# Kernel optimization log

Measured on AMD Instinct MI355X. Metric: run time of the kernel, lower is better.

The kernel has to match this reference:

```python
import jax, jax.numpy as jnp
import numpy as np

P = 16          # patch size
IMG = 224       # image size
EPS_COMBINE = 2.220446049250313e-16  # np.finfo(float).eps
NOISE_EPS = 0.01
LOSS_COEF = 1e-2
K = 1


def _patchify(x):
    # x: [B, C, H, W] -> [B, n_patches, C*P*P] (channel-major flatten, matching conv weight layout)
    B, C, H, W = x.shape
    gh, gw = H // P, W // P
    x = x.reshape(B, C, gh, P, gw, P)
    x = x.transpose(0, 2, 4, 1, 3, 5).reshape(B, gh * gw, C * P * P)
    return x


def _cv_squared(v):
    # squared coefficient of variation; torch .var() is unbiased (ddof=1)
    return jnp.var(v, ddof=1) / (jnp.mean(v) ** 2 + 1e-10)


def _norm_cdf(v):
    return jax.scipy.stats.norm.cdf(v)


def setup_inputs() -> dict:
    key = jax.random.key(0)
    ks = jax.random.split(key, 7)
    B, E, D_IN = 64, 8, 320
    x = jax.random.normal(ks[0], (B, 3, IMG, IMG), dtype=jnp.float32)
    g = jax.random.normal(ks[1], (B, D_IN), dtype=jnp.float32)
    noise = jax.random.normal(ks[2], (B, E), dtype=jnp.float32)
    w_gate = jax.random.normal(ks[3], (D_IN, E), dtype=jnp.float32) * 0.02
    w_noise = jax.random.normal(ks[4], (D_IN, E), dtype=jnp.float32) * 0.02
    w_exp = jax.random.normal(ks[5], (E, 768, 3, P, P), dtype=jnp.float32) * 0.02
    b_exp = jnp.zeros((E, 768), dtype=jnp.float32)
    return {"x": x, "g": g, "noise": noise, "w_gate": w_gate,
            "w_noise": w_noise, "w_exp": w_exp, "b_exp": b_exp}


def reference(x, g, noise, w_gate, w_noise, w_exp, b_exp):
    B = x.shape[0]
    E = w_gate.shape[1]

    # ---- noisy top-k gating (train mode) ----
    clean_logits = g @ w_gate                                   # [B, E]
    noise_stddev = jax.nn.softplus(g @ w_noise) + NOISE_EPS     # [B, E]
    noisy_logits = clean_logits + noise * noise_stddev          # [B, E]

    top_logits, top_idx = jax.lax.top_k(noisy_logits, K + 1)    # [B, K+1]
    top_k_gates = jax.nn.softmax(top_logits[:, :K], axis=1)     # [B, K]
    gates = jnp.zeros_like(noisy_logits).at[
        jnp.arange(B)[:, None], top_idx[:, :K]].set(top_k_gates)  # [B, E]

    # load: prob each expert's noisy logit lands in top-k (differentiable balance term)
    thr_in = top_logits[:, K][:, None]       # (k+1)-th value per row
    thr_out = top_logits[:, K - 1][:, None]  # k-th value per row
    is_in = noisy_logits > thr_in
    prob = jnp.where(is_in,
                     _norm_cdf((clean_logits - thr_in) / noise_stddev),
                     _norm_cdf((clean_logits - thr_out) / noise_stddev))
    load = prob.sum(0)                                           # [E]
    importance = gates.sum(0)                                    # [E]
    loss = (_cv_squared(importance) + _cv_squared(load)) * LOSS_COEF

    # ---- experts: per-expert patch-embed conv == patchify + GEMM ----
    patches = _patchify(x)                                       # [B, 196, 768]
    wf = w_exp.reshape(E, w_exp.shape[1], -1)                    # [E, out=768, in=768]
    y_exp = jnp.einsum('bpi,eoi->ebpo', patches, wf) + b_exp[:, None, None, :]  # [E,B,196,768]

    # ---- gate-weighted combine (dense equivalent of dispatch/combine) ----
    y = jnp.einsum('be,ebpo->bpo', gates, y_exp)                 # [B, 196, 768]
    y = jnp.where(y == 0, jnp.asarray(EPS_COMBINE, y.dtype), y)  # combined[combined==0] = eps
    return y, loss
```

## Files before the change

kernel.cpp:

```cpp
#include <hip/hip_runtime.h>
#include <math.h>

typedef unsigned short u16;
typedef unsigned int   u32;

using bf16x8 = __attribute__((ext_vector_type(8))) short;
using f32x4  = __attribute__((ext_vector_type(4))) float;

#define NB   64
#define NE   8
#define DIN  320
#define NP   196
#define CK   768
#define CN   768

#define BM 128
#define BN 128
#define BK 32
#define NKT (CK / BK)

#define WCONV_BLOCKS 2304

__device__ __forceinline__ u16 f2bf(float f) {
    u32 u = __builtin_bit_cast(u32, f);
    u += 0x7fffu + ((u >> 16) & 1u);
    return (u16)(u >> 16);
}

__device__ __forceinline__ u32 pkbf(float a, float b) {
    u32 ua = (__builtin_bit_cast(u32, a) + 0x8000u) >> 16;
    u32 ub = (__builtin_bit_cast(u32, b) + 0x8000u) & 0xffff0000u;
    return ua | ub;
}

__device__ __forceinline__ void gload16(const void* g, void* l) {
    __builtin_amdgcn_global_load_lds(
        (const __attribute__((address_space(1))) void*)g,
        (__attribute__((address_space(3))) void*)l, 16, 0, 0);
}

__global__ __launch_bounds__(256) void prep1_kernel(
    const float* __restrict__ g,
    const float* __restrict__ noise,
    const float* __restrict__ w_gate,
    const float* __restrict__ w_noise,
    const float* __restrict__ w_exp,
    float* __restrict__ gCl, float* __restrict__ gSd, float* __restrict__ gNy,
    u16* __restrict__ wb)
{
    __shared__ float sW[DIN][NE + 1];
    __shared__ float sWn[DIN][NE + 1];
    const int t = threadIdx.x;
    int bid = blockIdx.x;

    if (bid < 8) {
        for (int i = t; i < DIN * NE; i += 256) {
            sW[i >> 3][i & 7]  = w_gate[i];
            sWn[i >> 3][i & 7] = w_noise[i];
        }
        __syncthreads();
        const int pair = t >> 2, q = t & 3;
        const int bl = pair >> 3, e = pair & 7;
        const int b = bid * 8 + bl;
        float cl = 0.f, nz = 0.f;
        const float* gr = g + b * DIN + q * 80;
        #pragma unroll 4
        for (int j = 0; j < 80; ++j) {
            float gv = gr[j];
            cl = fmaf(gv, sW[q * 80 + j][e], cl);
            nz = fmaf(gv, sWn[q * 80 + j][e], nz);
        }
        cl += __shfl_xor(cl, 1); cl += __shfl_xor(cl, 2);
        nz += __shfl_xor(nz, 1); nz += __shfl_xor(nz, 2);
        if (q == 0) {
            int p = b * NE + e;
            float sd = fmaxf(nz, 0.f) + log1pf(expf(-fabsf(nz))) + 0.01f;
            gCl[p] = cl; gSd[p] = sd;
            gNy[p] = fmaf(noise[p], sd, cl);
        }
        return;
    }
    bid -= 8;
    int idx = bid * 256 + t;
    const float* src = w_exp + (size_t)idx * 8;
    float4 f0 = *reinterpret_cast<const float4*>(src);
    float4 f1 = *reinterpret_cast<const float4*>(src + 4);
    uint4 o;
    o.x = (u32)f2bf(f0.x) | ((u32)f2bf(f0.y) << 16);
    o.y = (u32)f2bf(f0.z) | ((u32)f2bf(f0.w) << 16);
    o.z = (u32)f2bf(f1.x) | ((u32)f2bf(f1.y) << 16);
    o.w = (u32)f2bf(f1.z) | ((u32)f2bf(f1.w) << 16);
    *reinterpret_cast<uint4*>(wb + (size_t)idx * 8) = o;
}

__global__ __launch_bounds__(512) void gate2_kernel(
    const float* __restrict__ gCl,
    const float* __restrict__ gSd,
    const float* __restrict__ gNy,
    int* __restrict__ eid,
    float* __restrict__ loss_out)
{
    __shared__ float sNy[NB][NE];
    __shared__ float sProb[NB][NE];
    __shared__ int   sTop[NB];
    __shared__ float sImp[NE], sLoad[NE];
    const int t = threadIdx.x;
    const int b = t >> 3, e = t & 7;
    float cl = gCl[t], sd = gSd[t], ny = gNy[t];
    sNy[b][e] = ny;
    __syncthreads();
    float v1 = -1e30f, v2 = -1e30f; int i1 = 0;
    #pragma unroll
    for (int k2 = 0; k2 < NE; ++k2) {
        float v = sNy[b][k2];
        if (v > v1) { v2 = v1; v1 = v; i1 = k2; }
        else if (v > v2) { v2 = v; }
    }
    if (e == 0) { sTop[b] = i1; eid[b] = i1; }
    float thr = (ny > v2) ? v2 : v1;
    float z = (cl - thr) / sd;
    sProb[b][e] = 0.5f * (1.0f + erff(z * 0.7071067811865476f));
    __syncthreads();
    if (t < NE) {
        float imp = 0.f, ld = 0.f;
        for (int i = 0; i < NB; ++i) {
            imp += (sTop[i] == t) ? 1.0f : 0.0f;
            ld  += sProb[i][t];
        }
        sImp[t] = imp; sLoad[t] = ld;
    }
    __syncthreads();
    if (t == 0) {
        float mi = 0.f, ml = 0.f;
        for (int k2 = 0; k2 < NE; ++k2) { mi += sImp[k2]; ml += sLoad[k2]; }
        mi *= (1.0f / NE); ml *= (1.0f / NE);
        float vi = 0.f, vl = 0.f;
        for (int k2 = 0; k2 < NE; ++k2) {
            float d1 = sImp[k2] - mi;  vi += d1 * d1;
            float d2 = sLoad[k2] - ml; vl += d2 * d2;
        }
        vi *= (1.0f / (NE - 1)); vl *= (1.0f / (NE - 1));
        loss_out[0] = (vi / (mi * mi + 1e-10f) + vl / (ml * ml + 1e-10f)) * 0.01f;
    }
}

__global__ __launch_bounds__(512) void gemm_kernel(
    const float* __restrict__ x,
    const u16* __restrict__ wb,
    const float* __restrict__ b_exp,
    const int* __restrict__ eid,
    float* __restrict__ out)
{
    __shared__ char smem[2][16384];

    const int id = blockIdx.x;
    const int v  = (id & 7) * 96 + (id >> 3);
    const int b  = v / 12;
    const int rr = v % 12;
    const int m0 = (rr / 6) * BM;
    const int n0 = (rr % 6) * BN;
    const int e  = eid[b];

    const int t  = threadIdx.x;
    const int l  = t & 63;
    const int w  = t >> 6;
    const int wm = w >> 1;
    const int wn = w & 1;

    const u32 cg = (u32)((l & 3) ^ (l >> 4));
    const u16* bS = wb + (size_t)e * (CK * CN)
                  + (size_t)(n0 + (w << 4) + (l >> 2)) * CK + cg * 8;
    const u32 bLds = 8192u + ((u32)w << 10) + ((u32)l << 4);

    const int arow = t >> 2;
    int p = m0 + arow; if (p > NP - 1) p = NP - 1;
    const int gh = p / 14, gw = p % 14;
    const int seg = (t & 3) >> 1, pw0 = (t & 1) * 8;
    const float* xb = x + (size_t)b * 150528 + (gh * 16 + seg) * 224 + gw * 16 + pw0;
    const u32 wA = (u32)(arow * 64 + (((t & 3) ^ ((arow >> 2) & 3)) << 4));

    u32 aOff[2], bOff[4];
    #pragma unroll
    for (int fm = 0; fm < 2; ++fm) {
        int row = wm * 32 + fm * 16 + (l & 15);
        aOff[fm] = (u32)(row * 64) + (((u32)(l >> 4) ^ (u32)((row >> 2) & 3)) << 4);
    }
    #pragma unroll
    for (int fn = 0; fn < 4; ++fn) {
        int row = wn * 64 + fn * 16 + (l & 15);
        bOff[fn] = 8192u + (u32)(row * 64) + (((u32)(l >> 4) ^ (u32)((row >> 2) & 3)) << 4);
    }

    f32x4 acc[2][4];
    #pragma unroll
    for (int fm = 0; fm < 2; ++fm)
        #pragma unroll
        for (int fn = 0; fn < 4; ++fn)
            acc[fm][fn] = (f32x4){0.f, 0.f, 0.f, 0.f};

    char* smem0 = &smem[0][0];

    {
        float4 ra0 = *reinterpret_cast<const float4*>(xb);
        float4 ra1 = *reinterpret_cast<const float4*>(xb + 4);
        __builtin_amdgcn_sched_barrier(0);
        gload16(bS, smem0 + bLds);
        __builtin_amdgcn_sched_barrier(0);
        uint4 o;
        o.x = pkbf(ra0.x, ra0.y); o.y = pkbf(ra0.z, ra0.w);
        o.z = pkbf(ra1.x, ra1.y); o.w = pkbf(ra1.z, ra1.w);
        *reinterpret_cast<uint4*>(smem0 + wA) = o;
        asm volatile("s_waitcnt lgkmcnt(0)" ::: "memory");
        __builtin_amdgcn_s_barrier();
    }

    for (int kt = 0; kt < NKT; ++kt) {
        const int kn = (kt + 1 < NKT) ? kt + 1 : NKT - 1;
        const int koff = (kn >> 3) * 50176 + (kn & 7) * 448;
        char* bufn = smem0 + (u32)(((kt + 1) & 1) * 16384);
        char* bufc = smem0 + (u32)((kt & 1) * 16384);

        float4 ra0 = *reinterpret_cast<const float4*>(xb + koff);
        float4 ra1 = *reinterpret_cast<const float4*>(xb + koff + 4);
        __builtin_amdgcn_sched_barrier(0);
        gload16(bS + kn * BK, bufn + bLds);
        __builtin_amdgcn_sched_barrier(0);
        asm volatile("s_waitcnt vmcnt(3)" ::: "memory");
        __builtin_amdgcn_s_barrier();

        bf16x8 af[2], bfr[4];
        #pragma unroll
        for (int fm = 0; fm < 2; ++fm)
            af[fm] = *reinterpret_cast<const bf16x8*>(bufc + aOff[fm]);
        #pragma unroll
        for (int fn = 0; fn < 4; ++fn)
            bfr[fn] = *reinterpret_cast<const bf16x8*>(bufc + bOff[fn]);

        #pragma unroll
        for (int fm = 0; fm < 2; ++fm)
            #pragma unroll
            for (int fn = 0; fn < 4; ++fn)
                acc[fm][fn] = __builtin_amdgcn_mfma_f32_16x16x32_bf16(
                    af[fm], bfr[fn], acc[fm][fn], 0, 0, 0);

        uint4 o;
        o.x = pkbf(ra0.x, ra0.y); o.y = pkbf(ra0.z, ra0.w);
        o.z = pkbf(ra1.x, ra1.y); o.w = pkbf(ra1.z, ra1.w);
        *reinterpret_cast<uint4*>(bufn + wA) = o;
        asm volatile("s_waitcnt lgkmcnt(0)" ::: "memory");
        __builtin_amdgcn_s_barrier();
    }

    const int r4 = (l >> 4) * 4;
    #pragma unroll
    for (int fm = 0; fm < 2; ++fm) {
        int mb = m0 + wm * 32 + fm * 16 + r4;
        #pragma unroll
        for (int fn = 0; fn < 4; ++fn) {
            int col = n0 + wn * 64 + fn * 16 + (l & 15);
            float bias = b_exp[e * CN + col];
            #pragma unroll
            for (int q = 0; q < 4; ++q) {
                int mrow = mb + q;
                if (mrow < NP) {
                    float vv = acc[fm][fn][q] + bias;
                    if (vv == 0.0f) vv = 2.220446049250313e-16f;
                    out[((size_t)b * NP + mrow) * CN + col] = vv;
                }
            }
        }
    }
}

extern "C" void kernel_launch(void* const* d_in, const int* in_sizes, int n_in,
                              void* d_out, int out_size, void* d_ws, size_t ws_size,
                              hipStream_t stream) {
    const float* x       = (const float*)d_in[0];
    const float* g       = (const float*)d_in[1];
    const float* noise   = (const float*)d_in[2];
    const float* w_gate  = (const float*)d_in[3];
    const float* w_noise = (const float*)d_in[4];
    const float* w_exp   = (const float*)d_in[5];
    const float* b_exp   = (const float*)d_in[6];
    float* out = (float*)d_out;

    char* ws = (char*)d_ws;
    int*   eid = (int*)ws;
    float* gCl = (float*)(ws + 256);
    float* gSd = (float*)(ws + 2304);
    float* gNy = (float*)(ws + 4352);
    u16*   wbf = (u16*)(ws + 8192);

    hipLaunchKernelGGL(prep1_kernel, dim3(8 + WCONV_BLOCKS), dim3(256), 0, stream,
                       g, noise, w_gate, w_noise, w_exp, gCl, gSd, gNy, wbf);
    hipLaunchKernelGGL(gate2_kernel, dim3(1), dim3(512), 0, stream,
                       gCl, gSd, gNy, eid, out + (size_t)NB * NP * CN);
    hipLaunchKernelGGL(gemm_kernel, dim3(CN / BN * (2 * NB)), dim3(512), 0, stream,
                       x, wbf, b_exp, eid, out);
}
```

Measured before the change: 58.01 us.

## Triple-buffer GEMM LDS pipeline with 256-thread blocks and larger per-wave tiles

The expert GEMM moves from 512 threads (8 waves, 32x64 per wave) to 256 threads (4 waves, 64x64 per wave). Each thread now loads two A rows and two B chunks per k-step. The double-buffered shared memory becomes a three-stage ring with a prefetch distance of two k-tiles, and the loop is unrolled by two with templated step variants for the tail. The aim is to hide global load latency better and raise MFMA work per LDS fragment load, at the cost of more registers per thread and more LDS per block (48KB, launch bounds of 3 blocks per CU).

```diff
diff --git a/kernel.cpp b/kernel.cpp
--- a/kernel.cpp
+++ b/kernel.cpp
@@ -144,14 +144,62 @@
     }
 }
 
-__global__ __launch_bounds__(512) void gemm_kernel(
+template<bool LOAD, bool WRITE, bool LAST>
+__device__ __forceinline__ void kstep(
+    char* sm, u32 bc, u32 bw, u32 bn, int kn,
+    const float* xc0, const float* xc1, u32 aw0, u32 aw1,
+    const u16* bS0, const u16* bS1, u32 bLds,
+    const u32 (&aOff)[4], const u32 (&bOff)[4],
+    float4 (&sL)[4], float4 (&sW)[4], f32x4 (&acc)[4][4])
+{
+    if constexpr (LAST) asm volatile("s_waitcnt vmcnt(0) lgkmcnt(0)" ::: "memory");
+    else                asm volatile("s_waitcnt vmcnt(6) lgkmcnt(0)" ::: "memory");
+    __builtin_amdgcn_s_barrier();
+    __builtin_amdgcn_sched_barrier(0);
+    if constexpr (LOAD) {
+        const int koff = (kn >> 3) * 50176 + (kn & 7) * 448;
+        sL[0] = *reinterpret_cast<const float4*>(xc0 + koff);
+        sL[1] = *reinterpret_cast<const float4*>(xc0 + koff + 4);
+        sL[2] = *reinterpret_cast<const float4*>(xc1 + koff);
+        sL[3] = *reinterpret_cast<const float4*>(xc1 + koff + 4);
+        __builtin_amdgcn_sched_barrier(0);
+        gload16(bS0 + kn * BK, sm + bn + 8192 + bLds);
+        gload16(bS1 + kn * BK, sm + bn + 8192 + bLds + 1024);
+        __builtin_amdgcn_sched_barrier(0);
+    }
+    bf16x8 af[4], bfr[4];
+    #pragma unroll
+    for (int fm = 0; fm < 4; ++fm)
+        af[fm] = *reinterpret_cast<const bf16x8*>(sm + bc + aOff[fm]);
+    #pragma unroll
+    for (int fn = 0; fn < 4; ++fn)
+        bfr[fn] = *reinterpret_cast<const bf16x8*>(sm + bc + 8192 + bOff[fn]);
+    #pragma unroll
+    for (int fm = 0; fm < 4; ++fm)
+        #pragma unroll
+        for (int fn = 0; fn < 4; ++fn)
+            acc[fm][fn] = __builtin_amdgcn_mfma_f32_16x16x32_bf16(
+                af[fm], bfr[fn], acc[fm][fn], 0, 0, 0);
+    if constexpr (WRITE) {
+        __builtin_amdgcn_sched_barrier(0);
+        uint4 o0, o1;
+        o0.x = pkbf(sW[0].x, sW[0].y); o0.y = pkbf(sW[0].z, sW[0].w);
+        o0.z = pkbf(sW[1].x, sW[1].y); o0.w = pkbf(sW[1].z, sW[1].w);
+        o1.x = pkbf(sW[2].x, sW[2].y); o1.y = pkbf(sW[2].z, sW[2].w);
+        o1.z = pkbf(sW[3].x, sW[3].y); o1.w = pkbf(sW[3].z, sW[3].w);
+        *reinterpret_cast<uint4*>(sm + bw + aw0) = o0;
+        *reinterpret_cast<uint4*>(sm + bw + aw1) = o1;
+    }
+}
+
+__global__ __launch_bounds__(256, 3) void gemm_kernel(
     const float* __restrict__ x,
     const u16* __restrict__ wb,
     const float* __restrict__ b_exp,
     const int* __restrict__ eid,
     float* __restrict__ out)
 {
-    __shared__ char smem[2][16384];
+    __shared__ char smem[3 * 16384];
 
     const int id = blockIdx.x;
     const int v  = (id & 7) * 96 + (id >> 3);
@@ -166,95 +214,95 @@
     const int w  = t >> 6;
     const int wm = w >> 1;
     const int wn = w & 1;
-
+    char* sm = smem;
+
+    const int rs = (w << 5) + (l >> 2);
     const u32 cg = (u32)((l & 3) ^ (l >> 4));
-    const u16* bS = wb + (size_t)e * (CK * CN)
-                  + (size_t)(n0 + (w << 4) + (l >> 2)) * CK + cg * 8;
-    const u32 bLds = 8192u + ((u32)w << 10) + ((u32)l << 4);
-
-    const int arow = t >> 2;
-    int p = m0 + arow; if (p > NP - 1) p = NP - 1;
-    const int gh = p / 14, gw = p % 14;
-    const int seg = (t & 3) >> 1, pw0 = (t & 1) * 8;
-    const float* xb = x + (size_t)b * 150528 + (gh * 16 + seg) * 224 + gw * 16 + pw0;
-    const u32 wA = (u32)(arow * 64 + (((t & 3) ^ ((arow >> 2) & 3)) << 4));
-
-    u32 aOff[2], bOff[4];
-    #pragma unroll
-    for (int fm = 0; fm < 2; ++fm) {
-        int row = wm * 32 + fm * 16 + (l & 15);
+    const u16* bS0 = wb + (size_t)e * (CK * CN) + (size_t)(n0 + rs) * CK + cg * 8;
+    const u16* bS1 = bS0 + (size_t)16 * CK;
+    const u32 bLds = ((u32)w << 11) + ((u32)l << 4);
+
+    u32 aw0, aw1;
+    const float *xc0, *xc1;
+    {
+        int gc = t;
+        int r = gc >> 2, cpr = gc & 3, s = (r >> 2) & 3;
+        int cg2 = cpr ^ s, seg = cg2 >> 1, px0 = (cg2 & 1) * 8;
+        int p = m0 + r; if (p > NP - 1) p = NP - 1;
+        xc0 = x + (size_t)b * 150528 + (p / 14 * 16 + seg) * 224 + (p % 14) * 16 + px0;
+        aw0 = (u32)(r * 64 + cpr * 16);
+        gc = t + 256;
+        r = gc >> 2; cpr = gc & 3; s = (r >> 2) & 3;
+        cg2 = cpr ^ s; seg = cg2 >> 1; px0 = (cg2 & 1) * 8;
+        p = m0 + r; if (p > NP - 1) p = NP - 1;
+        xc1 = x + (size_t)b * 150528 + (p / 14 * 16 + seg) * 224 + (p % 14) * 16 + px0;
+        aw1 = (u32)(r * 64 + cpr * 16);
+    }
+
+    u32 aOff[4], bOff[4];
+    #pragma unroll
+    for (int fm = 0; fm < 4; ++fm) {
+        int row = wm * 64 + fm * 16 + (l & 15);
         aOff[fm] = (u32)(row * 64) + (((u32)(l >> 4) ^ (u32)((row >> 2) & 3)) << 4);
     }
     #pragma unroll
     for (int fn = 0; fn < 4; ++fn) {
         int row = wn * 64 + fn * 16 + (l & 15);
-        bOff[fn] = 8192u + (u32)(row * 64) + (((u32)(l >> 4) ^ (u32)((row >> 2) & 3)) << 4);
-    }
-
-    f32x4 acc[2][4];
-    #pragma unroll
-    for (int fm = 0; fm < 2; ++fm)
+        bOff[fn] = (u32)(row * 64) + (((u32)(l >> 4) ^ (u32)((row >> 2) & 3)) << 4);
+    }
+
+    f32x4 acc[4][4];
+    #pragma unroll
+    for (int fm = 0; fm < 4; ++fm)
         #pragma unroll
         for (int fn = 0; fn < 4; ++fn)
             acc[fm][fn] = (f32x4){0.f, 0.f, 0.f, 0.f};
 
-    char* smem0 = &smem[0][0];
-
+    float4 sA0[4], sA1[4];
+
+    sA0[0] = *reinterpret_cast<const float4*>(xc0);
+    sA0[1] = *reinterpret_cast<const float4*>(xc0 + 4);
+    sA0[2] = *reinterpret_cast<const float4*>(xc1);
+    sA0[3] = *reinterpret_cast<const float4*>(xc1 + 4);
+    __builtin_amdgcn_sched_barrier(0);
+    gload16(bS0, sm + 8192 + bLds);
+    gload16(bS1, sm + 8192 + bLds + 1024);
+    __builtin_amdgcn_sched_barrier(0);
+    sA1[0] = *reinterpret_cast<const float4*>(xc0 + 448);
+    sA1[1] = *reinterpret_cast<const float4*>(xc0 + 448 + 4);
+    sA1[2] = *reinterpret_cast<const float4*>(xc1 + 448);
+    sA1[3] = *reinterpret_cast<const float4*>(xc1 + 448 + 4);
+    __builtin_amdgcn_sched_barrier(0);
+    gload16(bS0 + BK, sm + 16384 + 8192 + bLds);
+    gload16(bS1 + BK, sm + 16384 + 8192 + bLds + 1024);
+    __builtin_amdgcn_sched_barrier(0);
     {
-        float4 ra0 = *reinterpret_cast<const float4*>(xb);
-        float4 ra1 = *reinterpret_cast<const float4*>(xb + 4);
-        __builtin_amdgcn_sched_barrier(0);
-        gload16(bS, smem0 + bLds);
-        __builtin_amdgcn_sched_barrier(0);
-        uint4 o;
-        o.x = pkbf(ra0.x, ra0.y); o.y = pkbf(ra0.z, ra0.w);
-        o.z = pkbf(ra1.x, ra1.y); o.w = pkbf(ra1.z, ra1.w);
-        *reinterpret_cast<uint4*>(smem0 + wA) = o;
-        asm volatile("s_waitcnt lgkmcnt(0)" ::: "memory");
-        __builtin_amdgcn_s_barrier();
-    }
-
-    for (int kt = 0; kt < NKT; ++kt) {
-        const int kn = (kt + 1 < NKT) ? kt + 1 : NKT - 1;
-        const int koff = (kn >> 3) * 50176 + (kn & 7) * 448;
-        char* bufn = smem0 + (u32)(((kt + 1) & 1) * 16384);
-        char* bufc = smem0 + (u32)((kt & 1) * 16384);
-
-        float4 ra0 = *reinterpret_cast<const float4*>(xb + koff);
-        float4 ra1 = *reinterpret_cast<const float4*>(xb + koff + 4);
-        __builtin_amdgcn_sched_barrier(0);
-        gload16(bS + kn * BK, bufn + bLds);
-        __builtin_amdgcn_sched_barrier(0);
-        asm volatile("s_waitcnt vmcnt(3)" ::: "memory");
-        __builtin_amdgcn_s_barrier();
-
-        bf16x8 af[2], bfr[4];
-        #pragma unroll
-        for (int fm = 0; fm < 2; ++fm)
-            af[fm] = *reinterpret_cast<const bf16x8*>(bufc + aOff[fm]);
-        #pragma unroll
-        for (int fn = 0; fn < 4; ++fn)
-            bfr[fn] = *reinterpret_cast<const bf16x8*>(bufc + bOff[fn]);
-
-        #pragma unroll
-        for (int fm = 0; fm < 2; ++fm)
-            #pragma unroll
-            for (int fn = 0; fn < 4; ++fn)
-                acc[fm][fn] = __builtin_amdgcn_mfma_f32_16x16x32_bf16(
-                    af[fm], bfr[fn], acc[fm][fn], 0, 0, 0);
-
-        uint4 o;
-        o.x = pkbf(ra0.x, ra0.y); o.y = pkbf(ra0.z, ra0.w);
-        o.z = pkbf(ra1.x, ra1.y); o.w = pkbf(ra1.z, ra1.w);
-        *reinterpret_cast<uint4*>(bufn + wA) = o;
-        asm volatile("s_waitcnt lgkmcnt(0)" ::: "memory");
-        __builtin_amdgcn_s_barrier();
-    }
+        uint4 o0, o1;
+        o0.x = pkbf(sA0[0].x, sA0[0].y); o0.y = pkbf(sA0[0].z, sA0[0].w);
+        o0.z = pkbf(sA0[1].x, sA0[1].y); o0.w = pkbf(sA0[1].z, sA0[1].w);
+        o1.x = pkbf(sA0[2].x, sA0[2].y); o1.y = pkbf(sA0[2].z, sA0[2].w);
+        o1.z = pkbf(sA0[3].x, sA0[3].y); o1.w = pkbf(sA0[3].z, sA0[3].w);
+        *reinterpret_cast<uint4*>(sm + aw0) = o0;
+        *reinterpret_cast<uint4*>(sm + aw1) = o1;
+    }
+
+    u32 q0 = 0, q1 = 16384, q2 = 32768;
+    for (int kt = 0; kt < NKT - 2; kt += 2) {
+        kstep<true,  true, false>(sm, q0, q1, q2, kt + 2, xc0, xc1, aw0, aw1,
+                                  bS0, bS1, bLds, aOff, bOff, sA0, sA1, acc);
+        kstep<true,  true, false>(sm, q1, q2, q0, kt + 3, xc0, xc1, aw0, aw1,
+                                  bS0, bS1, bLds, aOff, bOff, sA1, sA0, acc);
+        u32 tq = q0; q0 = q2; q2 = q1; q1 = tq;
+    }
+    kstep<false, true, false>(sm, q0, q1, q2, 0, xc0, xc1, aw0, aw1,
+                              bS0, bS1, bLds, aOff, bOff, sA0, sA1, acc);
+    kstep<false, false, true>(sm, q1, q2, q0, 0, xc0, xc1, aw0, aw1,
+                              bS0, bS1, bLds, aOff, bOff, sA1, sA0, acc);
 
     const int r4 = (l >> 4) * 4;
     #pragma unroll
-    for (int fm = 0; fm < 2; ++fm) {
-        int mb = m0 + wm * 32 + fm * 16 + r4;
+    for (int fm = 0; fm < 4; ++fm) {
+        int mb = m0 + wm * 64 + fm * 16 + r4;
         #pragma unroll
         for (int fn = 0; fn < 4; ++fn) {
             int col = n0 + wn * 64 + fn * 16 + (l & 15);
@@ -295,6 +343,6 @@
                        g, noise, w_gate, w_noise, w_exp, gCl, gSd, gNy, wbf);
     hipLaunchKernelGGL(gate2_kernel, dim3(1), dim3(512), 0, stream,
                        gCl, gSd, gNy, eid, out + (size_t)NB * NP * CN);
-    hipLaunchKernelGGL(gemm_kernel, dim3(CN / BN * (2 * NB)), dim3(512), 0, stream,
+    hipLaunchKernelGGL(gemm_kernel, dim3(CN / BN * (2 * NB)), dim3(256), 0, stream,
                        x, wbf, b_exp, eid, out);
 }
```

Measured after the change: 57.51 us. About the same (-0.9%).

## Pre-patchify activations to bf16 and run LDS-free register-direct GEMM sorted by expert

Applied to the files above, without the earlier changes.

Adds a prep pass that converts x into a padded bf16 patch matrix. The GEMM now drops shared memory and loads MFMA fragments straight from global memory into registers, with a two-stage register double buffer, 4 waves of 64x64 tiles and setprio around the MFMA groups. The gate kernel builds a permutation that groups batches by chosen expert so blocks sharing the same weight slice run close together for better L2 reuse. The trade-offs are an extra HBM round trip for the patch buffer (never-written pad rows are read but their results are discarded) and uncoalesced 16-byte fragment loads without LDS reuse.

```diff
diff --git a/kernel.cpp b/kernel.cpp
--- a/kernel.cpp
+++ b/kernel.cpp
@@ -11,15 +11,14 @@
 #define NE   8
 #define DIN  320
 #define NP   196
+#define MPAD 256
 #define CK   768
 #define CN   768
-
-#define BM 128
-#define BN 128
-#define BK 32
-#define NKT (CK / BK)
-
-#define WCONV_BLOCKS 2304
+#define NKT  24
+
+#define GATE_BLOCKS  8
+#define WCONV_BLOCKS 1152
+#define PATCH_BLOCKS 2352
 
 __device__ __forceinline__ u16 f2bf(float f) {
     u32 u = __builtin_bit_cast(u32, f);
@@ -27,25 +26,15 @@
     return (u16)(u >> 16);
 }
 
-__device__ __forceinline__ u32 pkbf(float a, float b) {
-    u32 ua = (__builtin_bit_cast(u32, a) + 0x8000u) >> 16;
-    u32 ub = (__builtin_bit_cast(u32, b) + 0x8000u) & 0xffff0000u;
-    return ua | ub;
-}
-
-__device__ __forceinline__ void gload16(const void* g, void* l) {
-    __builtin_amdgcn_global_load_lds(
-        (const __attribute__((address_space(1))) void*)g,
-        (__attribute__((address_space(3))) void*)l, 16, 0, 0);
-}
-
 __global__ __launch_bounds__(256) void prep1_kernel(
+    const float* __restrict__ x,
     const float* __restrict__ g,
     const float* __restrict__ noise,
     const float* __restrict__ w_gate,
     const float* __restrict__ w_noise,
     const float* __restrict__ w_exp,
     float* __restrict__ gCl, float* __restrict__ gSd, float* __restrict__ gNy,
+    u16* __restrict__ patches,
     u16* __restrict__ wb)
 {
     __shared__ float sW[DIN][NE + 1];
@@ -53,7 +42,7 @@
     const int t = threadIdx.x;
     int bid = blockIdx.x;
 
-    if (bid < 8) {
+    if (bid < GATE_BLOCKS) {
         for (int i = t; i < DIN * NE; i += 256) {
             sW[i >> 3][i & 7]  = w_gate[i];
             sWn[i >> 3][i & 7] = w_noise[i];
@@ -80,17 +69,54 @@
         }
         return;
     }
-    bid -= 8;
+    bid -= GATE_BLOCKS;
+
+    if (bid < WCONV_BLOCKS) {
+        int idx = bid * 256 + t;
+        const float* src = w_exp + (size_t)idx * 16;
+        u16* dst = wb + (size_t)idx * 16;
+        float4 f0 = *reinterpret_cast<const float4*>(src);
+        float4 f1 = *reinterpret_cast<const float4*>(src + 4);
+        float4 f2 = *reinterpret_cast<const float4*>(src + 8);
+        float4 f3 = *reinterpret_cast<const float4*>(src + 12);
+        uint4 o0, o1;
+        o0.x = (u32)f2bf(f0.x) | ((u32)f2bf(f0.y) << 16);
+        o0.y = (u32)f2bf(f0.z) | ((u32)f2bf(f0.w) << 16);
+        o0.z = (u32)f2bf(f1.x) | ((u32)f2bf(f1.y) << 16);
+        o0.w = (u32)f2bf(f1.z) | ((u32)f2bf(f1.w) << 16);
+        o1.x = (u32)f2bf(f2.x) | ((u32)f2bf(f2.y) << 16);
+        o1.y = (u32)f2bf(f2.z) | ((u32)f2bf(f2.w) << 16);
+        o1.z = (u32)f2bf(f3.x) | ((u32)f2bf(f3.y) << 16);
+        o1.w = (u32)f2bf(f3.z) | ((u32)f2bf(f3.w) << 16);
+        *reinterpret_cast<uint4*>(dst)     = o0;
+        *reinterpret_cast<uint4*>(dst + 8) = o1;
+        return;
+    }
+    bid -= WCONV_BLOCKS;
+
     int idx = bid * 256 + t;
-    const float* src = w_exp + (size_t)idx * 8;
+    int ph = idx & 15;
+    int c  = (idx >> 4) % 3;
+    int p  = (idx / 48) % NP;
+    int b  = idx / (48 * NP);
+    int gh = p / 14, gw = p % 14;
+    const float* src = x + (((size_t)(b * 3 + c) * 224 + gh * 16 + ph) * 224 + gw * 16);
+    u16* dst = patches + ((size_t)(b * MPAD + p)) * CK + c * 256 + ph * 16;
     float4 f0 = *reinterpret_cast<const float4*>(src);
     float4 f1 = *reinterpret_cast<const float4*>(src + 4);
-    uint4 o;
-    o.x = (u32)f2bf(f0.x) | ((u32)f2bf(f0.y) << 16);
-    o.y = (u32)f2bf(f0.z) | ((u32)f2bf(f0.w) << 16);
-    o.z = (u32)f2bf(f1.x) | ((u32)f2bf(f1.y) << 16);
-    o.w = (u32)f2bf(f1.z) | ((u32)f2bf(f1.w) << 16);
-    *reinterpret_cast<uint4*>(wb + (size_t)idx * 8) = o;
+    float4 f2 = *reinterpret_cast<const float4*>(src + 8);
+    float4 f3 = *reinterpret_cast<const float4*>(src + 12);
+    uint4 o0, o1;
+    o0.x = (u32)f2bf(f0.x) | ((u32)f2bf(f0.y) << 16);
+    o0.y = (u32)f2bf(f0.z) | ((u32)f2bf(f0.w) << 16);
+    o0.z = (u32)f2bf(f1.x) | ((u32)f2bf(f1.y) << 16);
+    o0.w = (u32)f2bf(f1.z) | ((u32)f2bf(f1.w) << 16);
+    o1.x = (u32)f2bf(f2.x) | ((u32)f2bf(f2.y) << 16);
+    o1.y = (u32)f2bf(f2.z) | ((u32)f2bf(f2.w) << 16);
+    o1.z = (u32)f2bf(f3.x) | ((u32)f2bf(f3.y) << 16);
+    o1.w = (u32)f2bf(f3.z) | ((u32)f2bf(f3.w) << 16);
+    *reinterpret_cast<uint4*>(dst)     = o0;
+    *reinterpret_cast<uint4*>(dst + 8) = o1;
 }
 
 __global__ __launch_bounds__(512) void gate2_kernel(
@@ -98,6 +124,7 @@
     const float* __restrict__ gSd,
     const float* __restrict__ gNy,
     int* __restrict__ eid,
+    int* __restrict__ perm,
     float* __restrict__ loss_out)
 {
     __shared__ float sNy[NB][NE];
@@ -141,24 +168,27 @@
         }
         vi *= (1.0f / (NE - 1)); vl *= (1.0f / (NE - 1));
         loss_out[0] = (vi / (mi * mi + 1e-10f) + vl / (ml * ml + 1e-10f)) * 0.01f;
-    }
-}
-
-__global__ __launch_bounds__(512) void gemm_kernel(
-    const float* __restrict__ x,
-    const u16* __restrict__ wb,
+        int off[NE]; int s = 0;
+        #pragma unroll
+        for (int k2 = 0; k2 < NE; ++k2) { off[k2] = s; s += (int)sImp[k2]; }
+        for (int i = 0; i < NB; ++i) perm[off[sTop[i]]++] = i;
+    }
+}
+
+__global__ __launch_bounds__(256, 3) void gemm_kernel(
+    const u16* __restrict__ patches,
+    const u16* __restrict__ wbf,
     const float* __restrict__ b_exp,
     const int* __restrict__ eid,
+    const int* __restrict__ perm,
     float* __restrict__ out)
 {
-    __shared__ char smem[2][16384];
-
     const int id = blockIdx.x;
     const int v  = (id & 7) * 96 + (id >> 3);
-    const int b  = v / 12;
+    const int b  = perm[v / 12];
     const int rr = v % 12;
-    const int m0 = (rr / 6) * BM;
-    const int n0 = (rr % 6) * BN;
+    const int m0 = (rr / 6) * 128;
+    const int n0 = (rr % 6) * 128;
     const int e  = eid[b];
 
     const int t  = threadIdx.x;
@@ -166,95 +196,88 @@
     const int w  = t >> 6;
     const int wm = w >> 1;
     const int wn = w & 1;
-
-    const u32 cg = (u32)((l & 3) ^ (l >> 4));
-    const u16* bS = wb + (size_t)e * (CK * CN)
-                  + (size_t)(n0 + (w << 4) + (l >> 2)) * CK + cg * 8;
-    const u32 bLds = 8192u + ((u32)w << 10) + ((u32)l << 4);
-
-    const int arow = t >> 2;
-    int p = m0 + arow; if (p > NP - 1) p = NP - 1;
-    const int gh = p / 14, gw = p % 14;
-    const int seg = (t & 3) >> 1, pw0 = (t & 1) * 8;
-    const float* xb = x + (size_t)b * 150528 + (gh * 16 + seg) * 224 + gw * 16 + pw0;
-    const u32 wA = (u32)(arow * 64 + (((t & 3) ^ ((arow >> 2) & 3)) << 4));
-
-    u32 aOff[2], bOff[4];
-    #pragma unroll
-    for (int fm = 0; fm < 2; ++fm) {
-        int row = wm * 32 + fm * 16 + (l & 15);
-        aOff[fm] = (u32)(row * 64) + (((u32)(l >> 4) ^ (u32)((row >> 2) & 3)) << 4);
-    }
-    #pragma unroll
-    for (int fn = 0; fn < 4; ++fn) {
-        int row = wn * 64 + fn * 16 + (l & 15);
-        bOff[fn] = 8192u + (u32)(row * 64) + (((u32)(l >> 4) ^ (u32)((row >> 2) & 3)) << 4);
-    }
-
-    f32x4 acc[2][4];
-    #pragma unroll
-    for (int fm = 0; fm < 2; ++fm)
+    const int lr = l & 15;
+    const int lk = l >> 4;
+
+    const u16* aP[4];
+    const u16* bP[4];
+    #pragma unroll
+    for (int fm = 0; fm < 4; ++fm)
+        aP[fm] = patches + ((size_t)b * MPAD + m0 + wm * 64 + fm * 16 + lr) * CK + lk * 8;
+    #pragma unroll
+    for (int fn = 0; fn < 4; ++fn)
+        bP[fn] = wbf + (size_t)e * (CK * CN)
+               + (size_t)(n0 + wn * 64 + fn * 16 + lr) * CK + lk * 8;
+
+    f32x4 acc[4][4];
+    #pragma unroll
+    for (int fm = 0; fm < 4; ++fm)
         #pragma unroll
         for (int fn = 0; fn < 4; ++fn)
             acc[fm][fn] = (f32x4){0.f, 0.f, 0.f, 0.f};
 
-    char* smem0 = &smem[0][0];
-
-    {
-        float4 ra0 = *reinterpret_cast<const float4*>(xb);
-        float4 ra1 = *reinterpret_cast<const float4*>(xb + 4);
-        __builtin_amdgcn_sched_barrier(0);
-        gload16(bS, smem0 + bLds);
-        __builtin_amdgcn_sched_barrier(0);
-        uint4 o;
-        o.x = pkbf(ra0.x, ra0.y); o.y = pkbf(ra0.z, ra0.w);
-        o.z = pkbf(ra1.x, ra1.y); o.w = pkbf(ra1.z, ra1.w);
-        *reinterpret_cast<uint4*>(smem0 + wA) = o;
-        asm volatile("s_waitcnt lgkmcnt(0)" ::: "memory");
-        __builtin_amdgcn_s_barrier();
-    }
-
-    for (int kt = 0; kt < NKT; ++kt) {
-        const int kn = (kt + 1 < NKT) ? kt + 1 : NKT - 1;
-        const int koff = (kn >> 3) * 50176 + (kn & 7) * 448;
-        char* bufn = smem0 + (u32)(((kt + 1) & 1) * 16384);
-        char* bufc = smem0 + (u32)((kt & 1) * 16384);
-
-        float4 ra0 = *reinterpret_cast<const float4*>(xb + koff);
-        float4 ra1 = *reinterpret_cast<const float4*>(xb + koff + 4);
-        __builtin_amdgcn_sched_barrier(0);
-        gload16(bS + kn * BK, bufn + bLds);
-        __builtin_amdgcn_sched_barrier(0);
-        asm volatile("s_waitcnt vmcnt(3)" ::: "memory");
-        __builtin_amdgcn_s_barrier();
-
-        bf16x8 af[2], bfr[4];
-        #pragma unroll
-        for (int fm = 0; fm < 2; ++fm)
-            af[fm] = *reinterpret_cast<const bf16x8*>(bufc + aOff[fm]);
-        #pragma unroll
-        for (int fn = 0; fn < 4; ++fn)
-            bfr[fn] = *reinterpret_cast<const bf16x8*>(bufc + bOff[fn]);
-
-        #pragma unroll
-        for (int fm = 0; fm < 2; ++fm)
+    bf16x8 aE[4], bE[4], aO[4], bO[4];
+    #pragma unroll
+    for (int f = 0; f < 4; ++f) {
+        aE[f] = *reinterpret_cast<const bf16x8*>(aP[f]);
+        bE[f] = *reinterpret_cast<const bf16x8*>(bP[f]);
+    }
+
+    int kt = 0;
+    for (; kt < NKT - 2; kt += 2) {
+        #pragma unroll
+        for (int f = 0; f < 4; ++f) {
+            aO[f] = *reinterpret_cast<const bf16x8*>(aP[f] + (kt + 1) * 32);
+            bO[f] = *reinterpret_cast<const bf16x8*>(bP[f] + (kt + 1) * 32);
+        }
+        __builtin_amdgcn_s_setprio(1);
+        #pragma unroll
+        for (int fm = 0; fm < 4; ++fm)
             #pragma unroll
             for (int fn = 0; fn < 4; ++fn)
                 acc[fm][fn] = __builtin_amdgcn_mfma_f32_16x16x32_bf16(
-                    af[fm], bfr[fn], acc[fm][fn], 0, 0, 0);
-
-        uint4 o;
-        o.x = pkbf(ra0.x, ra0.y); o.y = pkbf(ra0.z, ra0.w);
-        o.z = pkbf(ra1.x, ra1.y); o.w = pkbf(ra1.z, ra1.w);
-        *reinterpret_cast<uint4*>(bufn + wA) = o;
-        asm volatile("s_waitcnt lgkmcnt(0)" ::: "memory");
-        __builtin_amdgcn_s_barrier();
+                    aE[fm], bE[fn], acc[fm][fn], 0, 0, 0);
+        __builtin_amdgcn_s_setprio(0);
+        #pragma unroll
+        for (int f = 0; f < 4; ++f) {
+            aE[f] = *reinterpret_cast<const bf16x8*>(aP[f] + (kt + 2) * 32);
+            bE[f] = *reinterpret_cast<const bf16x8*>(bP[f] + (kt + 2) * 32);
+        }
+        __builtin_amdgcn_s_setprio(1);
+        #pragma unroll
+        for (int fm = 0; fm < 4; ++fm)
+            #pragma unroll
+            for (int fn = 0; fn < 4; ++fn)
+                acc[fm][fn] = __builtin_amdgcn_mfma_f32_16x16x32_bf16(
+                    aO[fm], bO[fn], acc[fm][fn], 0, 0, 0);
+        __builtin_amdgcn_s_setprio(0);
+    }
+    {
+        #pragma unroll
+        for (int f = 0; f < 4; ++f) {
+            aO[f] = *reinterpret_cast<const bf16x8*>(aP[f] + (NKT - 1) * 32);
+            bO[f] = *reinterpret_cast<const bf16x8*>(bP[f] + (NKT - 1) * 32);
+        }
+        __builtin_amdgcn_s_setprio(1);
+        #pragma unroll
+        for (int fm = 0; fm < 4; ++fm)
+            #pragma unroll
+            for (int fn = 0; fn < 4; ++fn)
+                acc[fm][fn] = __builtin_amdgcn_mfma_f32_16x16x32_bf16(
+                    aE[fm], bE[fn], acc[fm][fn], 0, 0, 0);
+        #pragma unroll
+        for (int fm = 0; fm < 4; ++fm)
+            #pragma unroll
+            for (int fn = 0; fn < 4; ++fn)
+                acc[fm][fn] = __builtin_amdgcn_mfma_f32_16x16x32_bf16(
+                    aO[fm], bO[fn], acc[fm][fn], 0, 0, 0);
+        __builtin_amdgcn_s_setprio(0);
     }
 
     const int r4 = (l >> 4) * 4;
     #pragma unroll
-    for (int fm = 0; fm < 2; ++fm) {
-        int mb = m0 + wm * 32 + fm * 16 + r4;
+    for (int fm = 0; fm < 4; ++fm) {
+        int mb = m0 + wm * 64 + fm * 16 + r4;
         #pragma unroll
         for (int fn = 0; fn < 4; ++fn) {
             int col = n0 + wn * 64 + fn * 16 + (l & 15);
@@ -285,16 +308,19 @@
     float* out = (float*)d_out;
 
     char* ws = (char*)d_ws;
-    int*   eid = (int*)ws;
-    float* gCl = (float*)(ws + 256);
-    float* gSd = (float*)(ws + 2304);
-    float* gNy = (float*)(ws + 4352);
-    u16*   wbf = (u16*)(ws + 8192);
-
-    hipLaunchKernelGGL(prep1_kernel, dim3(8 + WCONV_BLOCKS), dim3(256), 0, stream,
-                       g, noise, w_gate, w_noise, w_exp, gCl, gSd, gNy, wbf);
+    int*   eid     = (int*)ws;
+    int*   perm    = (int*)(ws + 256);
+    float* gCl     = (float*)(ws + 512);
+    float* gSd     = (float*)(ws + 2560);
+    float* gNy     = (float*)(ws + 4608);
+    u16*   patches = (u16*)(ws + 8192);
+    u16*   wbf     = (u16*)(ws + 8192 + (size_t)NB * MPAD * CK * 2);
+
+    hipLaunchKernelGGL(prep1_kernel,
+                       dim3(GATE_BLOCKS + WCONV_BLOCKS + PATCH_BLOCKS), dim3(256), 0, stream,
+                       x, g, noise, w_gate, w_noise, w_exp, gCl, gSd, gNy, patches, wbf);
     hipLaunchKernelGGL(gate2_kernel, dim3(1), dim3(512), 0, stream,
-                       gCl, gSd, gNy, eid, out + (size_t)NB * NP * CN);
-    hipLaunchKernelGGL(gemm_kernel, dim3(CN / BN * (2 * NB)), dim3(512), 0, stream,
-                       x, wbf, b_exp, eid, out);
-}
+                       gCl, gSd, gNy, eid, perm, out + (size_t)NB * NP * CN);
+    hipLaunchKernelGGL(gemm_kernel, dim3(768), dim3(256), 0, stream,
+                       patches, wbf, b_exp, eid, perm, out);
+}
```

New measurement: 104.0 us. 79.2% more time.
